# Kernel optimization log

Hardware: AMD Instinct MI355X
Metric: run time of the kernel (lower is better)

The kernel has to match this reference:

```python
import jax, jax.numpy as jnp
import numpy as np

H = 512
W = 512


def setup_inputs() -> dict:
    key = jax.random.key(0)
    k1, k2 = jax.random.split(key)
    B, P, C = 8, 30000, 64
    pillar_features = jax.random.normal(k1, (B, P, C), dtype=jnp.float32)
    pillar_coords = jax.random.randint(k2, (B, P, 2), 0, 512, dtype=jnp.int32)
    return {"pillar_features": pillar_features, "pillar_coords": pillar_coords}


def _scatter_one(feat, coords):
    # feat: (P, C), coords: (P, 2) as [gx, gy]
    gx = coords[:, 0]
    gy = coords[:, 1]
    valid = (gx >= 0) & (gx < W) & (gy >= 0) & (gy < H)
    # invalid pillars -> out-of-range flat index, dropped by mode='drop'
    flat = jnp.where(valid, gy * W + gx, H * W)
    bev = jnp.zeros((H * W, feat.shape[1]), dtype=feat.dtype)
    bev = bev.at[flat].set(feat, mode="drop")
    # (H*W, C) -> (C, H, W)
    return bev.reshape(H, W, -1).transpose(2, 0, 1)


def reference(pillar_features, pillar_coords):
    return jax.vmap(_scatter_one)(pillar_features, pillar_coords)
```

## Files before the change

kernel.cpp:

```cpp
#include <hip/hip_runtime.h>

#define BEV_H 512
#define BEV_W 512
#define BEV_HW (BEV_H * BEV_W)
#define NB 8
#define NP 30000
#define NC 64

__global__ void scatter_winner_kernel(const int* __restrict__ coords,
                                      int* __restrict__ winner) {
    int idx = blockIdx.x * blockDim.x + threadIdx.x;
    if (idx >= NB * NP) return;
    int b = idx / NP;
    int p = idx - b * NP;
    int2 c2 = ((const int2*)coords)[idx];
    int gx = c2.x;
    int gy = c2.y;
    if (gx >= 0 && gx < BEV_W && gy >= 0 && gy < BEV_H) {
        atomicMax(&winner[b * BEV_HW + gy * BEV_W + gx], p);
    }
}

__global__ void gather_out_kernel(const float* __restrict__ feat,
                                  const int* __restrict__ winner,
                                  float* __restrict__ out) {
    int bc = blockIdx.y;
    int b  = bc >> 6;
    int c  = bc & (NC - 1);
    int cell = (blockIdx.x * blockDim.x + threadIdx.x) << 2;

    const int4 w4 = *(const int4*)(winner + (size_t)b * BEV_HW + cell);
    const float* fb = feat + (size_t)b * NP * NC + c;

    float4 v;
    v.x = (w4.x >= 0) ? fb[(size_t)w4.x * NC] : 0.0f;
    v.y = (w4.y >= 0) ? fb[(size_t)w4.y * NC] : 0.0f;
    v.z = (w4.z >= 0) ? fb[(size_t)w4.z * NC] : 0.0f;
    v.w = (w4.w >= 0) ? fb[(size_t)w4.w * NC] : 0.0f;

    *(float4*)(out + (size_t)bc * BEV_HW + cell) = v;
}

extern "C" void kernel_launch(void* const* d_in, const int* in_sizes, int n_in,
                              void* d_out, int out_size, void* d_ws, size_t ws_size,
                              hipStream_t stream) {
    const float* feat   = (const float*)d_in[0];
    const int*   coords = (const int*)d_in[1];
    float*       out    = (float*)d_out;
    int*         winner = (int*)d_ws;

    hipMemsetAsync(winner, 0xFF, (size_t)NB * BEV_HW * sizeof(int), stream);

    {
        int total = NB * NP;
        int block = 256;
        int grid  = (total + block - 1) / block;
        scatter_winner_kernel<<<grid, block, 0, stream>>>(coords, winner);
    }

    {
        dim3 block(256, 1, 1);
        dim3 grid(BEV_HW / (4 * 256), NB * NC, 1);
        gather_out_kernel<<<grid, block, 0, stream>>>(feat, winner, out);
    }
}
```

Measured before the change: 596.6 us.

## Gather whole pillar feature rows per cell and transpose in registers

```diff
diff --git a/kernel.cpp b/kernel.cpp
--- a/kernel.cpp
+++ b/kernel.cpp
@@ -21,24 +21,39 @@
     }
 }
 
-__global__ void gather_out_kernel(const float* __restrict__ feat,
-                                  const int* __restrict__ winner,
-                                  float* __restrict__ out) {
-    int bc = blockIdx.y;
-    int b  = bc >> 6;
-    int c  = bc & (NC - 1);
-    int cell = (blockIdx.x * blockDim.x + threadIdx.x) << 2;
+__global__ void __launch_bounds__(256)
+gather_out_kernel(const float* __restrict__ feat,
+                  const int* __restrict__ winner,
+                  float* __restrict__ out) {
+    const int b    = blockIdx.y;
+    const int cell = (blockIdx.x * blockDim.x + threadIdx.x) << 2;
 
     const int4 w4 = *(const int4*)(winner + (size_t)b * BEV_HW + cell);
-    const float* fb = feat + (size_t)b * NP * NC + c;
 
-    float4 v;
-    v.x = (w4.x >= 0) ? fb[(size_t)w4.x * NC] : 0.0f;
-    v.y = (w4.y >= 0) ? fb[(size_t)w4.y * NC] : 0.0f;
-    v.z = (w4.z >= 0) ? fb[(size_t)w4.z * NC] : 0.0f;
-    v.w = (w4.w >= 0) ? fb[(size_t)w4.w * NC] : 0.0f;
+    const float* __restrict__ fb = feat + (size_t)b * NP * NC;
+    const float* __restrict__ r0 = fb + (size_t)(w4.x < 0 ? 0 : w4.x) * NC;
+    const float* __restrict__ r1 = fb + (size_t)(w4.y < 0 ? 0 : w4.y) * NC;
+    const float* __restrict__ r2 = fb + (size_t)(w4.z < 0 ? 0 : w4.z) * NC;
+    const float* __restrict__ r3 = fb + (size_t)(w4.w < 0 ? 0 : w4.w) * NC;
 
-    *(float4*)(out + (size_t)bc * BEV_HW + cell) = v;
+    float* __restrict__ ob = out + (size_t)b * NC * BEV_HW + cell;
+
+    #pragma unroll 2
+    for (int c0 = 0; c0 < NC; c0 += 4) {
+        float4 va = *(const float4*)(r0 + c0);
+        float4 vb = *(const float4*)(r1 + c0);
+        float4 vc = *(const float4*)(r2 + c0);
+        float4 vd = *(const float4*)(r3 + c0);
+        if (w4.x < 0) va = make_float4(0.f, 0.f, 0.f, 0.f);
+        if (w4.y < 0) vb = make_float4(0.f, 0.f, 0.f, 0.f);
+        if (w4.z < 0) vc = make_float4(0.f, 0.f, 0.f, 0.f);
+        if (w4.w < 0) vd = make_float4(0.f, 0.f, 0.f, 0.f);
+
+        *(float4*)(ob + (size_t)(c0 + 0) * BEV_HW) = make_float4(va.x, vb.x, vc.x, vd.x);
+        *(float4*)(ob + (size_t)(c0 + 1) * BEV_HW) = make_float4(va.y, vb.y, vc.y, vd.y);
+        *(float4*)(ob + (size_t)(c0 + 2) * BEV_HW) = make_float4(va.z, vb.z, vc.z, vd.z);
+        *(float4*)(ob + (size_t)(c0 + 3) * BEV_HW) = make_float4(va.w, vb.w, vc.w, vd.w);
+    }
 }
 
 extern "C" void kernel_launch(void* const* d_in, const int* in_sizes, int n_in,
@@ -60,7 +75,7 @@
 
     {
         dim3 block(256, 1, 1);
-        dim3 grid(BEV_HW / (4 * 256), NB * NC, 1);
+        dim3 grid(BEV_HW / (4 * 256), NB, 1);
         gather_out_kernel<<<grid, block, 0, stream>>>(feat, winner, out);
     }
 }
```

New measurement: 665.9 us. 11.6% more time.

## Gather 16 channels per thread with vectorized feature row loads

Applied to the files above, without the earlier changes.

```diff
diff --git a/kernel.cpp b/kernel.cpp
--- a/kernel.cpp
+++ b/kernel.cpp
@@ -21,24 +21,50 @@
     }
 }
 
-__global__ void gather_out_kernel(const float* __restrict__ feat,
-                                  const int* __restrict__ winner,
-                                  float* __restrict__ out) {
-    int bc = blockIdx.y;
-    int b  = bc >> 6;
-    int c  = bc & (NC - 1);
-    int cell = (blockIdx.x * blockDim.x + threadIdx.x) << 2;
+__global__ void __launch_bounds__(256)
+gather_out_kernel(const float* __restrict__ feat,
+                  const int* __restrict__ winner,
+                  float* __restrict__ out) {
+    const int b    = blockIdx.y >> 2;
+    const int g    = blockIdx.y & 3;
+    const int cell = (blockIdx.x * blockDim.x + threadIdx.x) << 2;
 
     const int4 w4 = *(const int4*)(winner + (size_t)b * BEV_HW + cell);
-    const float* fb = feat + (size_t)b * NP * NC + c;
+    const int w[4] = {w4.x, w4.y, w4.z, w4.w};
 
-    float4 v;
-    v.x = (w4.x >= 0) ? fb[(size_t)w4.x * NC] : 0.0f;
-    v.y = (w4.y >= 0) ? fb[(size_t)w4.y * NC] : 0.0f;
-    v.z = (w4.z >= 0) ? fb[(size_t)w4.z * NC] : 0.0f;
-    v.w = (w4.w >= 0) ? fb[(size_t)w4.w * NC] : 0.0f;
+    const float* __restrict__ fb = feat + (size_t)b * NP * NC + g * 16;
 
-    *(float4*)(out + (size_t)bc * BEV_HW + cell) = v;
+    float4 v[4][4];
+    #pragma unroll
+    for (int k = 0; k < 4; ++k) {
+        const float* __restrict__ rk = fb + (size_t)(w[k] < 0 ? 0 : w[k]) * NC;
+        #pragma unroll
+        for (int j = 0; j < 4; ++j)
+            v[k][j] = *(const float4*)(rk + 4 * j);
+    }
+
+    #pragma unroll
+    for (int k = 0; k < 4; ++k) {
+        if (w[k] < 0) {
+            #pragma unroll
+            for (int j = 0; j < 4; ++j)
+                v[k][j] = make_float4(0.f, 0.f, 0.f, 0.f);
+        }
+    }
+
+    float* __restrict__ ob =
+        out + (size_t)b * NC * BEV_HW + (size_t)(g * 16) * BEV_HW + cell;
+    #pragma unroll
+    for (int j = 0; j < 4; ++j) {
+        *(float4*)(ob + (size_t)(4 * j + 0) * BEV_HW) =
+            make_float4(v[0][j].x, v[1][j].x, v[2][j].x, v[3][j].x);
+        *(float4*)(ob + (size_t)(4 * j + 1) * BEV_HW) =
+            make_float4(v[0][j].y, v[1][j].y, v[2][j].y, v[3][j].y);
+        *(float4*)(ob + (size_t)(4 * j + 2) * BEV_HW) =
+            make_float4(v[0][j].z, v[1][j].z, v[2][j].z, v[3][j].z);
+        *(float4*)(ob + (size_t)(4 * j + 3) * BEV_HW) =
+            make_float4(v[0][j].w, v[1][j].w, v[2][j].w, v[3][j].w);
+    }
 }
 
 extern "C" void kernel_launch(void* const* d_in, const int* in_sizes, int n_in,
@@ -60,7 +86,7 @@
 
     {
         dim3 block(256, 1, 1);
-        dim3 grid(BEV_HW / (4 * 256), NB * NC, 1);
+        dim3 grid(BEV_HW / (4 * 256), NB * 4, 1);
         gather_out_kernel<<<grid, block, 0, stream>>>(feat, winner, out);
     }
 }
```

Result: no change. 587.1 us (-1.6%).
